# Optimization experiments

Measured on AMD Instinct MI355X. Metric: run time of the kernel, lower is better.

The kernel has to match this reference:

```python
import jax, jax.numpy as jnp
import numpy as np

N = 50000      # nodes
E = 800000     # edges
DIN = 128      # input_dim
FN = 128       # filter_num
OUT = 16       # out_dim (classes)
K = 10         # APPNP power-iteration steps
ALPHA = 0.1    # teleport probability


def _glorot_linear(key, fan_in, fan_out):
    s = 1.0 / np.sqrt(fan_in)
    kw, kb = jax.random.split(key)
    W = jax.random.uniform(kw, (fan_in, fan_out), jnp.float32, -s, s)
    b = jax.random.uniform(kb, (fan_out,), jnp.float32, -s, s)
    return W, b


def setup_inputs() -> dict:
    key = jax.random.key(0)
    ks = jax.random.split(key, 6)
    x = jax.random.normal(ks[0], (N, DIN), jnp.float32)
    edge_index = jax.random.randint(ks[1], (2, E), 0, N, dtype=jnp.int64)
    W1, b1 = _glorot_linear(ks[2], DIN, FN)
    W2, b2 = _glorot_linear(ks[3], FN, FN)
    W3, b3 = _glorot_linear(ks[4], FN, FN)
    Wc, bc = _glorot_linear(ks[5], FN, OUT)  # Conv1d kernel_size=1 == per-node linear
    return {"x": x, "edge_index": edge_index, "W1": W1, "b1": b1,
            "W2": W2, "b2": b2, "W3": W3, "b3": b3, "Wc": Wc, "bc": bc}


def _appnp(x, row, col, w, n):
    # x_{k+1} = (1-alpha) * A_hat @ x_k + alpha * x_0
    h = x
    def step(xk, _):
        msg = w[:, None] * xk[row]                      # [E+N, F] gather
        agg = jax.ops.segment_sum(msg, col, num_segments=n)  # scatter-add SpMM
        return (1.0 - ALPHA) * agg + ALPHA * h, None
    out, _ = jax.lax.scan(step, x, None, length=K)
    return out


def reference(x, edge_index, W1, b1, W2, b2, W3, b3, Wc, bc):
    n = x.shape[0]
    # gcn_norm with self-loops: w_e = deg(col)^-1/2 * deg(row)^-1/2
    loops = jnp.arange(n, dtype=edge_index.dtype)
    row = jnp.concatenate([edge_index[0], loops])
    col = jnp.concatenate([edge_index[1], loops])
    deg = jax.ops.segment_sum(jnp.ones_like(col, x.dtype), col, num_segments=n)
    dinv = jnp.where(deg > 0, jax.lax.rsqrt(deg), 0.0)
    w = dinv[row] * dinv[col]

    h = jax.nn.relu(_appnp(x @ W1 + b1, row, col, w, n))
    h = jax.nn.relu(_appnp(h @ W2 + b2, row, col, w, n))
    h = jax.nn.relu(_appnp(h @ W3 + b3, row, col, w, n))
    logits = h @ Wc + bc                                # 1x1 Conv1d == linear
    return jax.nn.log_softmax(logits, axis=1)
```

## Files before the change

kernel.cpp:

```cpp
#include <hip/hip_runtime.h>
#include <math.h>

#define FD 128
#define NOUT 16
#define ALPHA_F 0.1f

typedef short short8 __attribute__((ext_vector_type(8)));
typedef float f32x4 __attribute__((ext_vector_type(4)));

__device__ __forceinline__ float bflo(unsigned u) { return __uint_as_float(u << 16); }
__device__ __forceinline__ float bfhi(unsigned u) { return __uint_as_float(u & 0xffff0000u); }
__device__ __forceinline__ unsigned f2bf(float f) {
    unsigned u = __float_as_uint(f);
    u += 0x7fffu + ((u >> 16) & 1u);
    return u >> 16;
}
__device__ __forceinline__ unsigned pack2(float a, float b) {
    return f2bf(a) | (f2bf(b) << 16);
}


__global__ void count_kernel(const int* __restrict__ cols, int* __restrict__ cnt, int e) {
    int i = blockIdx.x * blockDim.x + threadIdx.x;
    if (i < e) atomicAdd(&cnt[cols[i]], 1);
}

__global__ void dinv_kernel(const int* __restrict__ cnt, float* __restrict__ dinv, int n) {
    int i = blockIdx.x * blockDim.x + threadIdx.x;
    if (i < n) dinv[i] = rsqrtf((float)(cnt[i] + 1));
}

__device__ __forceinline__ int padded(int cnt) { return (cnt + 8) & ~7; }

__global__ void scan_partial_kernel(const int* __restrict__ cnt, int* __restrict__ bsum, int n) {
    __shared__ int sh[256];
    int base = blockIdx.x * 1024 + threadIdx.x * 4;
    int s = 0;
    #pragma unroll
    for (int j = 0; j < 4; ++j) { int i = base + j; if (i < n) s += padded(cnt[i]); }
    sh[threadIdx.x] = s; __syncthreads();
    for (int d = 128; d > 0; d >>= 1) {
        if ((int)threadIdx.x < d) sh[threadIdx.x] += sh[threadIdx.x + d];
        __syncthreads();
    }
    if (threadIdx.x == 0) bsum[blockIdx.x] = sh[0];
}

__global__ void scan_base_kernel(int* __restrict__ bsum, int* __restrict__ off, int nb, int n) {
    if (threadIdx.x == 0 && blockIdx.x == 0) {
        int run = 0;
        for (int b = 0; b < nb; ++b) { int t = bsum[b]; bsum[b] = run; run += t; }
        off[n] = run;
    }
}

__global__ void scan_final_kernel(const int* __restrict__ cnt, const int* __restrict__ bsum,
                                  int* __restrict__ off, int* __restrict__ cur, int n) {
    __shared__ int sh[256];
    int t = threadIdx.x;
    int base_i = blockIdx.x * 1024 + t * 4;
    int v[4]; int s = 0;
    #pragma unroll
    for (int j = 0; j < 4; ++j) { int i = base_i + j; v[j] = (i < n) ? padded(cnt[i]) : 0; s += v[j]; }
    sh[t] = s; __syncthreads();
    for (int d = 1; d < 256; d <<= 1) {
        int x = (t >= d) ? sh[t - d] : 0;
        __syncthreads();
        sh[t] += x;
        __syncthreads();
    }
    int excl = sh[t] - s + bsum[blockIdx.x];
    #pragma unroll
    for (int j = 0; j < 4; ++j) {
        int i = base_i + j;
        if (i < n) { off[i] = excl; cur[i] = excl; }
        excl += v[j];
    }
}

__global__ void fill_edges_kernel(const int* __restrict__ rows, const int* __restrict__ cols,
                                  const float* __restrict__ dinv, int* __restrict__ cur,
                                  unsigned* __restrict__ eg, int e) {
    int i = blockIdx.x * blockDim.x + threadIdx.x;
    if (i < e) {
        int r = rows[i];
        int c = cols[i];
        int pos = atomicAdd(&cur[c], 1);
        eg[pos] = (f2bf(dinv[r] * dinv[c]) << 16) | (unsigned)r;
    }
}

__global__ void fill_loops_kernel(const float* __restrict__ dinv, int* __restrict__ cur,
                                  unsigned* __restrict__ eg, int n) {
    int i = blockIdx.x * blockDim.x + threadIdx.x;
    if (i < n) {
        int pos = atomicAdd(&cur[i], 1);
        eg[pos] = (f2bf(dinv[i] * dinv[i]) << 16) | (unsigned)i;
    }
}


__global__ void wtrans_kernel(const float* __restrict__ W, unsigned* __restrict__ Wt) {
    int idx = blockIdx.x * 256 + threadIdx.x;
    if (idx < 128 * 64) {
        int c = idx >> 6, ku = idx & 63;
        Wt[idx] = pack2(W[(2 * ku) * FD + c], W[(2 * ku + 1) * FD + c]);
    }
}

template <int BF_IN>
__global__ __launch_bounds__(256, 4)
void gemm_mfma_kernel(const void* __restrict__ Xv, const unsigned* __restrict__ Wt,
                      const float* __restrict__ bias,
                      unsigned* __restrict__ Ab, unsigned* __restrict__ Z0b, int n) {
    int l = threadIdx.x & 63;
    int w = threadIdx.x >> 6;
    int l15 = l & 15, lq = l >> 4;
    int r0 = blockIdx.x * 64 + w * 16;
    int arow = min(r0 + l15, n - 1);
    const unsigned* bptr = Wt + (size_t)l15 * 64 + lq * 4;

    f32x4 acc[8];
    #pragma unroll
    for (int nt = 0; nt < 8; ++nt) acc[nt] = (f32x4){0.f, 0.f, 0.f, 0.f};

    #pragma unroll
    for (int kk = 0; kk < 4; ++kk) {
        short8 af;
        if (BF_IN) {
            const unsigned* aptr = (const unsigned*)Xv + (size_t)arow * 64 + lq * 4;
            af = *(const short8*)(aptr + kk * 16);
        } else {
            const float* ap = (const float*)Xv + (size_t)arow * FD + lq * 8 + kk * 32;
            float4 fa = *(const float4*)(ap);
            float4 fb = *(const float4*)(ap + 4);
            unsigned p0 = pack2(fa.x, fa.y), p1 = pack2(fa.z, fa.w);
            unsigned p2 = pack2(fb.x, fb.y), p3 = pack2(fb.z, fb.w);
            uint4 u = make_uint4(p0, p1, p2, p3);
            af = *(const short8*)&u;
        }
        #pragma unroll
        for (int nt = 0; nt < 8; ++nt) {
            short8 bf = *(const short8*)(bptr + nt * 1024 + kk * 16);
            acc[nt] = __builtin_amdgcn_mfma_f32_16x16x32_bf16(af, bf, acc[nt], 0, 0, 0);
        }
    }

    #pragma unroll
    for (int nt = 0; nt < 8; ++nt) {
        float b_ = bias[nt * 16 + l15];
        #pragma unroll
        for (int j = 0; j < 4; ++j) {
            float v = acc[nt][j] + b_;
            float vp = __shfl_xor(v, 1);
            int row = r0 + lq * 4 + j;
            if (!(l & 1) && row < n) {
                int cu = nt * 8 + (l15 >> 1);
                Ab[(size_t)row * 64 + cu]  = pack2(v, vp);
                Z0b[(size_t)row * 64 + cu] = pack2(ALPHA_F * v, ALPHA_F * vp);
            }
        }
    }
}

__global__ __launch_bounds__(256, 8)
void spmm_bf16_kernel(const int* __restrict__ off, const unsigned* __restrict__ eg,
                      const unsigned* __restrict__ Xin, const unsigned* __restrict__ X0b,
                      unsigned* __restrict__ Xout, int n, int relu) {
    int node = blockIdx.x * 8 + ((int)threadIdx.x >> 5);
    if (node >= n) return;
    int lane31 = threadIdx.x & 31;
    int s = off[node];
    int degpad = off[node + 1] - s;
    int dother = __shfl_xor(degpad, 32);
    int dm = max(degpad, dother);
    const uint2* Xg = (const uint2*)Xin;
    uint2 x0 = ((const uint2*)X0b)[node * 32 + lane31];
    float a0 = 0.f, a1 = 0.f, a2 = 0.f, a3 = 0.f;

    for (int base = 0; base < dm; base += 8) {
        int p = s + min(base, degpad - 8);
        bool live = base < degpad;
        uint4 ra = *(const uint4*)(eg + p);
        uint4 rb = *(const uint4*)(eg + p + 4);
        uint2 g0 = Xg[(ra.x & 0xffffu) * 32 + lane31];
        uint2 g1 = Xg[(ra.y & 0xffffu) * 32 + lane31];
        uint2 g2 = Xg[(ra.z & 0xffffu) * 32 + lane31];
        uint2 g3 = Xg[(ra.w & 0xffffu) * 32 + lane31];
        uint2 g4 = Xg[(rb.x & 0xffffu) * 32 + lane31];
        uint2 g5 = Xg[(rb.y & 0xffffu) * 32 + lane31];
        uint2 g6 = Xg[(rb.z & 0xffffu) * 32 + lane31];
        uint2 g7 = Xg[(rb.w & 0xffffu) * 32 + lane31];
        float w0 = live ? bfhi(ra.x) : 0.f;
        float w1 = live ? bfhi(ra.y) : 0.f;
        float w2 = live ? bfhi(ra.z) : 0.f;
        float w3 = live ? bfhi(ra.w) : 0.f;
        float w4 = live ? bfhi(rb.x) : 0.f;
        float w5 = live ? bfhi(rb.y) : 0.f;
        float w6 = live ? bfhi(rb.z) : 0.f;
        float w7 = live ? bfhi(rb.w) : 0.f;
        a0 += w0 * bflo(g0.x); a1 += w0 * bfhi(g0.x); a2 += w0 * bflo(g0.y); a3 += w0 * bfhi(g0.y);
        a0 += w1 * bflo(g1.x); a1 += w1 * bfhi(g1.x); a2 += w1 * bflo(g1.y); a3 += w1 * bfhi(g1.y);
        a0 += w2 * bflo(g2.x); a1 += w2 * bfhi(g2.x); a2 += w2 * bflo(g2.y); a3 += w2 * bfhi(g2.y);
        a0 += w3 * bflo(g3.x); a1 += w3 * bfhi(g3.x); a2 += w3 * bflo(g3.y); a3 += w3 * bfhi(g3.y);
        a0 += w4 * bflo(g4.x); a1 += w4 * bfhi(g4.x); a2 += w4 * bflo(g4.y); a3 += w4 * bfhi(g4.y);
        a0 += w5 * bflo(g5.x); a1 += w5 * bfhi(g5.x); a2 += w5 * bflo(g5.y); a3 += w5 * bfhi(g5.y);
        a0 += w6 * bflo(g6.x); a1 += w6 * bfhi(g6.x); a2 += w6 * bflo(g6.y); a3 += w6 * bfhi(g6.y);
        a0 += w7 * bflo(g7.x); a1 += w7 * bfhi(g7.x); a2 += w7 * bflo(g7.y); a3 += w7 * bfhi(g7.y);
    }

    float v0 = 0.9f * a0 + bflo(x0.x);
    float v1 = 0.9f * a1 + bfhi(x0.x);
    float v2 = 0.9f * a2 + bflo(x0.y);
    float v3 = 0.9f * a3 + bfhi(x0.y);
    if (relu) {
        v0 = fmaxf(v0, 0.f); v1 = fmaxf(v1, 0.f);
        v2 = fmaxf(v2, 0.f); v3 = fmaxf(v3, 0.f);
    }
    ((uint2*)Xout)[node * 32 + lane31] = make_uint2(pack2(v0, v1), pack2(v2, v3));
}

__global__ void head_kernel(const unsigned* __restrict__ Hb, const float* __restrict__ Wc,
                            const float* __restrict__ bc, float* __restrict__ out, int n) {
    int t = threadIdx.x;
    int o = t & (NOUT - 1);
    int node = blockIdx.x * (256 / NOUT) + (t >> 4);
    if (node >= n) return;
    float acc = bc[o];
    const uint4* hrow = (const uint4*)(Hb + (size_t)node * 64);
    #pragma unroll 4
    for (int k4 = 0; k4 < 16; ++k4) {
        uint4 u = hrow[k4];
        int k = k4 * 8;
        acc += bflo(u.x) * Wc[(k + 0) * NOUT + o];
        acc += bfhi(u.x) * Wc[(k + 1) * NOUT + o];
        acc += bflo(u.y) * Wc[(k + 2) * NOUT + o];
        acc += bfhi(u.y) * Wc[(k + 3) * NOUT + o];
        acc += bflo(u.z) * Wc[(k + 4) * NOUT + o];
        acc += bfhi(u.z) * Wc[(k + 5) * NOUT + o];
        acc += bflo(u.w) * Wc[(k + 6) * NOUT + o];
        acc += bfhi(u.w) * Wc[(k + 7) * NOUT + o];
    }
    float m = acc;
    #pragma unroll
    for (int d = NOUT / 2; d > 0; d >>= 1) m = fmaxf(m, __shfl_xor(m, d, NOUT));
    float ex = __expf(acc - m);
    float s = ex;
    #pragma unroll
    for (int d = NOUT / 2; d > 0; d >>= 1) s += __shfl_xor(s, d, NOUT);
    out[node * NOUT + o] = acc - m - __logf(s);
}


static inline size_t align256(size_t x) { return (x + 255) & ~(size_t)255; }

extern "C" void kernel_launch(void* const* d_in, const int* in_sizes, int n_in,
                              void* d_out, int out_size, void* d_ws, size_t ws_size,
                              hipStream_t stream) {
    const float* x  = (const float*)d_in[0];
    const int*   ei = (const int*)d_in[1];
    const float* W1 = (const float*)d_in[2];
    const float* b1 = (const float*)d_in[3];
    const float* W2 = (const float*)d_in[4];
    const float* b2 = (const float*)d_in[5];
    const float* W3 = (const float*)d_in[6];
    const float* b3 = (const float*)d_in[7];
    const float* Wc = (const float*)d_in[8];
    const float* bc = (const float*)d_in[9];
    float* out = (float*)d_out;

    const int n = in_sizes[0] / FD;
    const int e = in_sizes[1] / 2;
    const int nnz_max = e + n + 8 * n + 16;
    const int nb = (n + 1023) / 1024;

    const int* rows = ei;
    const int* cols = ei + e;

    char* p = (char*)d_ws;
    int*      off  = (int*)p;       p += align256((size_t)(n + 1) * 4);
    int*      cur  = (int*)p;       p += align256((size_t)n * 4);
    float*    dinv = (float*)p;     p += align256((size_t)n * 4);
    int*      bsum = (int*)p;       p += align256((size_t)nb * 4);
    unsigned* eg   = (unsigned*)p;  p += align256((size_t)nnz_max * 4);
    unsigned* Wt   = (unsigned*)p;  p += align256((size_t)3 * 8192 * 4);
    unsigned* Ab   = (unsigned*)p;  p += align256((size_t)n * 64 * 4);
    unsigned* Bb   = (unsigned*)p;  p += align256((size_t)n * 64 * 4);
    unsigned* Z0b  = (unsigned*)p;  p += align256((size_t)n * 64 * 4);
    unsigned* Hb   = (unsigned*)p;  p += align256((size_t)n * 64 * 4);

    hipMemsetAsync(cur, 0, (size_t)n * 4, stream);
    hipMemsetAsync(eg, 0, (size_t)nnz_max * 4, stream);
    count_kernel<<<(e + 255) / 256, 256, 0, stream>>>(cols, cur, e);
    dinv_kernel<<<(n + 255) / 256, 256, 0, stream>>>(cur, dinv, n);
    scan_partial_kernel<<<nb, 256, 0, stream>>>(cur, bsum, n);
    scan_base_kernel<<<1, 64, 0, stream>>>(bsum, off, nb, n);
    scan_final_kernel<<<nb, 256, 0, stream>>>(cur, bsum, off, cur, n);
    fill_edges_kernel<<<(e + 255) / 256, 256, 0, stream>>>(rows, cols, dinv, cur, eg, e);
    fill_loops_kernel<<<(n + 255) / 256, 256, 0, stream>>>(dinv, cur, eg, n);

    wtrans_kernel<<<32, 256, 0, stream>>>(W1, Wt);
    wtrans_kernel<<<32, 256, 0, stream>>>(W2, Wt + 8192);
    wtrans_kernel<<<32, 256, 0, stream>>>(W3, Wt + 16384);

    const int gemm_grid = (n + 63) / 64;
    const int spmm_grid = (n + 7) / 8;
    const float* bl[3] = { b1, b2, b3 };
    const void* gin = x;

    for (int st = 0; st < 3; ++st) {
        if (st == 0)
            gemm_mfma_kernel<0><<<gemm_grid, 256, 0, stream>>>(gin, Wt, bl[st], Ab, Z0b, n);
        else
            gemm_mfma_kernel<1><<<gemm_grid, 256, 0, stream>>>(gin, Wt + st * 8192, bl[st], Ab, Z0b, n);
        unsigned* bufs[2] = { Ab, Bb };
        int cu = 0;
        for (int k = 0; k < 10; ++k) {
            unsigned* o_ = (k == 9) ? Hb : bufs[cu ^ 1];
            spmm_bf16_kernel<<<spmm_grid, 256, 0, stream>>>(off, eg, bufs[cu], Z0b, o_, n, k == 9);
            cu ^= 1;
        }
        gin = Hb;
    }

    head_kernel<<<(n + 15) / 16, 256, 0, stream>>>(Hb, Wc, bc, out, n);
}
```

Measured before the change: 1.110 ms.

## Split feature matrix into four 32-column planes for cache-friendly SpMM gathers

Stores the bf16 node features as four column planes (each n×32 features) instead of row-major 128-wide rows, and assigns SpMM blocks to a single plane so that the gathered working set per plane is a quarter of the full matrix and fits better in L2/MALL. GEMM and head kernels are updated to read and write the planar layout. Edge-list loads and the output store now use nontemporal hints, and the per-half-wave max-degree padding is dropped. In exchange, the edge list and offsets are re-read four times, and each gather moves only 64 bytes per node per plane.

Result: slower. 1.477 ms (+33.0%).

```diff
diff --git a/kernel.cpp b/kernel.cpp
--- a/kernel.cpp
+++ b/kernel.cpp
@@ -7,6 +7,7 @@
 
 typedef short short8 __attribute__((ext_vector_type(8)));
 typedef float f32x4 __attribute__((ext_vector_type(4)));
+typedef unsigned uintx4 __attribute__((ext_vector_type(4)));
 
 __device__ __forceinline__ float bflo(unsigned u) { return __uint_as_float(u << 16); }
 __device__ __forceinline__ float bfhi(unsigned u) { return __uint_as_float(u & 0xffff0000u); }
@@ -17,6 +18,15 @@
 }
 __device__ __forceinline__ unsigned pack2(float a, float b) {
     return f2bf(a) | (f2bf(b) << 16);
+}
+__device__ __forceinline__ uintx4 ntload4(const unsigned* p) {
+    return __builtin_nontemporal_load((const uintx4*)p);
+}
+__device__ __forceinline__ unsigned ntload1(const unsigned* p) {
+    return __builtin_nontemporal_load(p);
+}
+__device__ __forceinline__ void ntstore1(unsigned* p, unsigned v) {
+    __builtin_nontemporal_store(v, p);
 }
 
 
@@ -119,6 +129,7 @@
     int r0 = blockIdx.x * 64 + w * 16;
     int arow = min(r0 + l15, n - 1);
     const unsigned* bptr = Wt + (size_t)l15 * 64 + lq * 4;
+    const size_t pstride = (size_t)n * 16;
 
     f32x4 acc[8];
     #pragma unroll
@@ -128,8 +139,9 @@
     for (int kk = 0; kk < 4; ++kk) {
         short8 af;
         if (BF_IN) {
-            const unsigned* aptr = (const unsigned*)Xv + (size_t)arow * 64 + lq * 4;
-            af = *(const short8*)(aptr + kk * 16);
+            const unsigned* aptr = (const unsigned*)Xv + (size_t)kk * pstride
+                                   + (size_t)arow * 16 + lq * 4;
+            af = *(const short8*)aptr;
         } else {
             const float* ap = (const float*)Xv + (size_t)arow * FD + lq * 8 + kk * 32;
             float4 fa = *(const float4*)(ap);
@@ -156,68 +168,58 @@
             int row = r0 + lq * 4 + j;
             if (!(l & 1) && row < n) {
                 int cu = nt * 8 + (l15 >> 1);
-                Ab[(size_t)row * 64 + cu]  = pack2(v, vp);
-                Z0b[(size_t)row * 64 + cu] = pack2(ALPHA_F * v, ALPHA_F * vp);
+                size_t idx = (size_t)(cu >> 4) * pstride + (size_t)row * 16 + (cu & 15);
+                Ab[idx]  = pack2(v, vp);
+                Z0b[idx] = pack2(ALPHA_F * v, ALPHA_F * vp);
             }
         }
     }
 }
 
 __global__ __launch_bounds__(256, 8)
-void spmm_bf16_kernel(const int* __restrict__ off, const unsigned* __restrict__ eg,
-                      const unsigned* __restrict__ Xin, const unsigned* __restrict__ X0b,
-                      unsigned* __restrict__ Xout, int n, int relu) {
-    int node = blockIdx.x * 8 + ((int)threadIdx.x >> 5);
+void spmm_plane_kernel(const int* __restrict__ off, const unsigned* __restrict__ eg,
+                       const unsigned* __restrict__ Xin, const unsigned* __restrict__ X0b,
+                       unsigned* __restrict__ Xout, int n, int relu) {
+    int b = blockIdx.x;
+    int plane = b & 3;
+    int node = (b >> 2) * 16 + ((int)threadIdx.x >> 4);
     if (node >= n) return;
-    int lane31 = threadIdx.x & 31;
+    int j = threadIdx.x & 15;
+    const size_t pbase = (size_t)plane * n * 16;
+    const unsigned* Xp = Xin + pbase;
     int s = off[node];
     int degpad = off[node + 1] - s;
-    int dother = __shfl_xor(degpad, 32);
-    int dm = max(degpad, dother);
-    const uint2* Xg = (const uint2*)Xin;
-    uint2 x0 = ((const uint2*)X0b)[node * 32 + lane31];
-    float a0 = 0.f, a1 = 0.f, a2 = 0.f, a3 = 0.f;
-
-    for (int base = 0; base < dm; base += 8) {
-        int p = s + min(base, degpad - 8);
-        bool live = base < degpad;
-        uint4 ra = *(const uint4*)(eg + p);
-        uint4 rb = *(const uint4*)(eg + p + 4);
-        uint2 g0 = Xg[(ra.x & 0xffffu) * 32 + lane31];
-        uint2 g1 = Xg[(ra.y & 0xffffu) * 32 + lane31];
-        uint2 g2 = Xg[(ra.z & 0xffffu) * 32 + lane31];
-        uint2 g3 = Xg[(ra.w & 0xffffu) * 32 + lane31];
-        uint2 g4 = Xg[(rb.x & 0xffffu) * 32 + lane31];
-        uint2 g5 = Xg[(rb.y & 0xffffu) * 32 + lane31];
-        uint2 g6 = Xg[(rb.z & 0xffffu) * 32 + lane31];
-        uint2 g7 = Xg[(rb.w & 0xffffu) * 32 + lane31];
-        float w0 = live ? bfhi(ra.x) : 0.f;
-        float w1 = live ? bfhi(ra.y) : 0.f;
-        float w2 = live ? bfhi(ra.z) : 0.f;
-        float w3 = live ? bfhi(ra.w) : 0.f;
-        float w4 = live ? bfhi(rb.x) : 0.f;
-        float w5 = live ? bfhi(rb.y) : 0.f;
-        float w6 = live ? bfhi(rb.z) : 0.f;
-        float w7 = live ? bfhi(rb.w) : 0.f;
-        a0 += w0 * bflo(g0.x); a1 += w0 * bfhi(g0.x); a2 += w0 * bflo(g0.y); a3 += w0 * bfhi(g0.y);
-        a0 += w1 * bflo(g1.x); a1 += w1 * bfhi(g1.x); a2 += w1 * bflo(g1.y); a3 += w1 * bfhi(g1.y);
-        a0 += w2 * bflo(g2.x); a1 += w2 * bfhi(g2.x); a2 += w2 * bflo(g2.y); a3 += w2 * bfhi(g2.y);
-        a0 += w3 * bflo(g3.x); a1 += w3 * bfhi(g3.x); a2 += w3 * bflo(g3.y); a3 += w3 * bfhi(g3.y);
-        a0 += w4 * bflo(g4.x); a1 += w4 * bfhi(g4.x); a2 += w4 * bflo(g4.y); a3 += w4 * bfhi(g4.y);
-        a0 += w5 * bflo(g5.x); a1 += w5 * bfhi(g5.x); a2 += w5 * bflo(g5.y); a3 += w5 * bfhi(g5.y);
-        a0 += w6 * bflo(g6.x); a1 += w6 * bfhi(g6.x); a2 += w6 * bflo(g6.y); a3 += w6 * bfhi(g6.y);
-        a0 += w7 * bflo(g7.x); a1 += w7 * bfhi(g7.x); a2 += w7 * bflo(g7.y); a3 += w7 * bfhi(g7.y);
-    }
-
-    float v0 = 0.9f * a0 + bflo(x0.x);
-    float v1 = 0.9f * a1 + bfhi(x0.x);
-    float v2 = 0.9f * a2 + bflo(x0.y);
-    float v3 = 0.9f * a3 + bfhi(x0.y);
-    if (relu) {
-        v0 = fmaxf(v0, 0.f); v1 = fmaxf(v1, 0.f);
-        v2 = fmaxf(v2, 0.f); v3 = fmaxf(v3, 0.f);
-    }
-    ((uint2*)Xout)[node * 32 + lane31] = make_uint2(pack2(v0, v1), pack2(v2, v3));
+    unsigned x0 = ntload1(X0b + pbase + (size_t)node * 16 + j);
+    const unsigned* ep = eg + s;
+    float a0 = 0.f, a1 = 0.f;
+
+    for (int c = 0; c < degpad; c += 8) {
+        uintx4 ra = ntload4(ep + c);
+        uintx4 rb = ntload4(ep + c + 4);
+        unsigned g0 = Xp[(ra[0] & 0xffffu) * 16u + j];
+        unsigned g1 = Xp[(ra[1] & 0xffffu) * 16u + j];
+        unsigned g2 = Xp[(ra[2] & 0xffffu) * 16u + j];
+        unsigned g3 = Xp[(ra[3] & 0xffffu) * 16u + j];
+        unsigned g4 = Xp[(rb[0] & 0xffffu) * 16u + j];
+        unsigned g5 = Xp[(rb[1] & 0xffffu) * 16u + j];
+        unsigned g6 = Xp[(rb[2] & 0xffffu) * 16u + j];
+        unsigned g7 = Xp[(rb[3] & 0xffffu) * 16u + j];
+        float w0 = bfhi(ra[0]), w1 = bfhi(ra[1]), w2 = bfhi(ra[2]), w3 = bfhi(ra[3]);
+        float w4 = bfhi(rb[0]), w5 = bfhi(rb[1]), w6 = bfhi(rb[2]), w7 = bfhi(rb[3]);
+        a0 += w0 * bflo(g0); a1 += w0 * bfhi(g0);
+        a0 += w1 * bflo(g1); a1 += w1 * bfhi(g1);
+        a0 += w2 * bflo(g2); a1 += w2 * bfhi(g2);
+        a0 += w3 * bflo(g3); a1 += w3 * bfhi(g3);
+        a0 += w4 * bflo(g4); a1 += w4 * bfhi(g4);
+        a0 += w5 * bflo(g5); a1 += w5 * bfhi(g5);
+        a0 += w6 * bflo(g6); a1 += w6 * bfhi(g6);
+        a0 += w7 * bflo(g7); a1 += w7 * bfhi(g7);
+    }
+
+    float v0 = 0.9f * a0 + bflo(x0);
+    float v1 = 0.9f * a1 + bfhi(x0);
+    if (relu) { v0 = fmaxf(v0, 0.f); v1 = fmaxf(v1, 0.f); }
+    ntstore1(Xout + pbase + (size_t)node * 16 + j, pack2(v0, v1));
 }
 
 __global__ void head_kernel(const unsigned* __restrict__ Hb, const float* __restrict__ Wc,
@@ -226,20 +228,24 @@
     int o = t & (NOUT - 1);
     int node = blockIdx.x * (256 / NOUT) + (t >> 4);
     if (node >= n) return;
+    const size_t pstride = (size_t)n * 16;
     float acc = bc[o];
-    const uint4* hrow = (const uint4*)(Hb + (size_t)node * 64);
-    #pragma unroll 4
-    for (int k4 = 0; k4 < 16; ++k4) {
-        uint4 u = hrow[k4];
-        int k = k4 * 8;
-        acc += bflo(u.x) * Wc[(k + 0) * NOUT + o];
-        acc += bfhi(u.x) * Wc[(k + 1) * NOUT + o];
-        acc += bflo(u.y) * Wc[(k + 2) * NOUT + o];
-        acc += bfhi(u.y) * Wc[(k + 3) * NOUT + o];
-        acc += bflo(u.z) * Wc[(k + 4) * NOUT + o];
-        acc += bfhi(u.z) * Wc[(k + 5) * NOUT + o];
-        acc += bflo(u.w) * Wc[(k + 6) * NOUT + o];
-        acc += bfhi(u.w) * Wc[(k + 7) * NOUT + o];
+    #pragma unroll
+    for (int p = 0; p < 4; ++p) {
+        const uint4* hp = (const uint4*)(Hb + (size_t)p * pstride + (size_t)node * 16);
+        #pragma unroll
+        for (int q = 0; q < 4; ++q) {
+            uint4 u = hp[q];
+            int k = p * 32 + q * 8;
+            acc += bflo(u.x) * Wc[(k + 0) * NOUT + o];
+            acc += bfhi(u.x) * Wc[(k + 1) * NOUT + o];
+            acc += bflo(u.y) * Wc[(k + 2) * NOUT + o];
+            acc += bfhi(u.y) * Wc[(k + 3) * NOUT + o];
+            acc += bflo(u.z) * Wc[(k + 4) * NOUT + o];
+            acc += bfhi(u.z) * Wc[(k + 5) * NOUT + o];
+            acc += bflo(u.w) * Wc[(k + 6) * NOUT + o];
+            acc += bfhi(u.w) * Wc[(k + 7) * NOUT + o];
+        }
     }
     float m = acc;
     #pragma unroll
@@ -304,7 +310,7 @@
     wtrans_kernel<<<32, 256, 0, stream>>>(W3, Wt + 16384);
 
     const int gemm_grid = (n + 63) / 64;
-    const int spmm_grid = (n + 7) / 8;
+    const int spmm_grid = ((n + 15) / 16) * 4;
     const float* bl[3] = { b1, b2, b3 };
     const void* gin = x;
 
@@ -317,7 +323,7 @@
         int cu = 0;
         for (int k = 0; k < 10; ++k) {
             unsigned* o_ = (k == 9) ? Hb : bufs[cu ^ 1];
-            spmm_bf16_kernel<<<spmm_grid, 256, 0, stream>>>(off, eg, bufs[cu], Z0b, o_, n, k == 9);
+            spmm_plane_kernel<<<spmm_grid, 256, 0, stream>>>(off, eg, bufs[cu], Z0b, o_, n, k == 9);
             cu ^= 1;
         }
         gin = Hb;
```
